# Performance work log

Measured on AMD Instinct MI355X. Metric: run time of the kernel, lower is better.

The kernel has to match this reference:

```python
import jax, jax.numpy as jnp
import numpy as np

EPS = 1e-8
LN_EPS = 1e-5
B, T, VDIM, ADIM, DM = 8, 2048, 1024, 768, 256
HID = 1024  # max(64, min(4*256, 2048))
DELTA_LOW, DELTA_HIGH = 2.0, 6.0
WINDOW = 5.0
GATE_MIN, GATE_MAX = 0.05, 0.95


def layer_norm(x):
    mu = jnp.mean(x, axis=-1, keepdims=True)
    var = jnp.var(x, axis=-1, keepdims=True)
    return (x - mu) / jnp.sqrt(var + LN_EPS)


def l2_normalize(x):
    n = jnp.sqrt(jnp.sum(x * x, axis=-1, keepdims=True))
    return x / jnp.maximum(n, EPS)


def setup_inputs() -> dict:
    key = jax.random.key(0)
    ks = jax.random.split(key, 8)
    inp = {
        "video_seq": jax.random.normal(ks[0], (B, T, VDIM), jnp.float32),
        "audio_seq": jax.random.normal(ks[1], (B, T, ADIM), jnp.float32),
        "Wv": jax.random.normal(ks[2], (VDIM, DM), jnp.float32) * (1.0 / np.sqrt(VDIM)),
        "bv": jnp.zeros((DM,), jnp.float32),
        "Wa": jax.random.normal(ks[3], (ADIM, DM), jnp.float32) * (1.0 / np.sqrt(ADIM)),
        "ba": jnp.zeros((DM,), jnp.float32),
        "theta": jnp.float32(0.0),
        "W1": jax.random.normal(ks[4], (3 * DM, HID), jnp.float32) * (1.0 / np.sqrt(3 * DM)),
        "b1": jnp.zeros((HID,), jnp.float32),
        "W2": jax.random.normal(ks[5], (HID, 1), jnp.float32) * (1.0 / np.sqrt(HID)),
        "b2": jnp.zeros((1,), jnp.float32),
    }
    return inp


def reference(video_seq, audio_seq, Wv, bv, Wa, ba, theta, W1, b1, W2, b2):
    v = layer_norm(video_seq @ Wv + bv)          # [B,T,DM]
    a = layer_norm(audio_seq @ Wa + ba)          # [B,T,DM]
    b, t, d = v.shape

    # LearnableDelay
    th = jnp.clip(theta, -12.0, 12.0)
    delta = DELTA_LOW + (DELTA_HIGH - DELTA_LOW) * jax.nn.sigmoid(th)
    delta_b = jnp.full((b,), delta, jnp.float32)

    # SoftTemporalShift (right shift with linear interpolation)
    dl = jnp.clip(delta_b, 0.0, float(t - 1))[:, None, None]   # [B,1,1]
    n = jnp.floor(dl)
    alpha = dl - n
    n_i = n.astype(jnp.int32)
    tidx = jnp.arange(t, dtype=jnp.int32)[None, :, None]       # [1,T,1]
    idx0 = jnp.clip(tidx - n_i, 0, t - 1)                      # [B,T,1]
    idx1 = jnp.clip(idx0 + 1, 0, t - 1)
    a0 = jnp.take_along_axis(a, jnp.broadcast_to(idx0, (b, t, d)), axis=1)
    a1 = jnp.take_along_axis(a, jnp.broadcast_to(idx1, (b, t, d)), axis=1)
    a_shift = (1.0 - alpha) * a0 + alpha * a1

    # DisplacementAwareCausalMask (hard, single scale)
    tf = jnp.arange(t, dtype=jnp.float32)
    tt = tf[None, :, None]                                     # t  -> [1,T,1]
    tau = tf[None, None, :]                                    # tau -> [1,1,T]
    center = jnp.minimum(jnp.maximum(tt + delta_b[:, None, None], 0.0), tt)
    raw = (jnp.abs(tau - center) <= WINDOW).astype(jnp.float32)
    raw = raw * (tau <= tt).astype(jnp.float32)
    M = raw / jnp.maximum(jnp.sum(raw, axis=-1, keepdims=True), EPS)  # [B,T,T]

    # mask-weighted audio context
    a_ctx = jnp.einsum('btk,bkd->btd', M, a_shift)

    # AlignmentGate (dropout inactive at eval)
    vn = l2_normalize(v)
    an = l2_normalize(a_ctx)
    x = jnp.concatenate([an, vn, an * vn], axis=-1)            # [B,T,3*DM]
    h = jax.nn.gelu(x @ W1 + b1, approximate=False)
    logits = jnp.clip(h @ W2 + b2, -12.0, 12.0)                # [B,T,1]
    g = jnp.clip(jax.nn.sigmoid(logits), GATE_MIN, GATE_MAX)

    fused = g * a_ctx + (1.0 - g) * v                          # [B,T,DM]
    return fused
```

## Files before the change

### kernel.cpp

```cpp
#include <hip/hip_runtime.h>
#include <cstdint>
#include <cstddef>

typedef unsigned short u16;
typedef unsigned int u32;
typedef __attribute__((ext_vector_type(8))) short short8;
typedef __attribute__((ext_vector_type(4))) float f32x4;

#define T_SEQ 2048
#define BT_ROWS 16384

__device__ __forceinline__ u16 f2bf(float x) {
  union { float f; u32 u; } v; v.f = x;
  u32 r = v.u + 0x7fffu + ((v.u >> 16) & 1u);
  return (u16)(r >> 16);
}
__device__ __forceinline__ u32 pkbf(float lo, float hi) {
  union { float f; u32 u; } a, b; a.f = lo; b.f = hi;
  const u32 ra = a.u + 0x7fffu + ((a.u >> 16) & 1u);
  const u32 rb = b.u + 0x7fffu + ((b.u >> 16) & 1u);
  return __builtin_amdgcn_perm(rb, ra, 0x07060302);
}
__device__ __forceinline__ float wave_bcast_sum(float x) {
#pragma unroll
  for (int off = 32; off > 0; off >>= 1) x += __shfl_down(x, off);
  return __shfl(x, 0);
}
__device__ __forceinline__ void gl_lds16(const void* g, void* l) {
  __builtin_amdgcn_global_load_lds((const __attribute__((address_space(1))) u32*)g,
                                   (__attribute__((address_space(3))) u32*)l, 16, 0, 0);
}
__device__ __forceinline__ float gelu_f(float x) {
  float z = 1.5957691216057308f * x * (1.0f + 0.044715f * x * x);
  float e = __expf(z);
  return x - x * __builtin_amdgcn_rcpf(1.0f + e);
}

__global__ __launch_bounds__(256) void tcvt_all(const float* __restrict__ Wv,
                                                const float* __restrict__ Wa,
                                                const float* __restrict__ W1,
                                                u16* __restrict__ wvT,
                                                u16* __restrict__ waT,
                                                u16* __restrict__ w1T,
                                                float* __restrict__ logits) {
  int b = blockIdx.x;
  if (b >= 1216) {
    logits[(b - 1216) * 256 + threadIdx.x] = 0.0f;
    return;
  }
  __shared__ float tile[32][33];
  const float* in; u16* out; int K, N, bx, by;
  if (b < 256)      { in = Wv; out = wvT; K = 1024; N = 256;  bx = b & 31;  by = b >> 5; }
  else if (b < 448) { b -= 256; in = Wa; out = waT; K = 768; N = 256;  bx = b % 24; by = b / 24; }
  else              { b -= 448; in = W1; out = w1T; K = 768; N = 1024; bx = b % 24; by = b / 24; }
  const int k0 = bx * 32, n0 = by * 32;
  const int tx = threadIdx.x & 31, ty = threadIdx.x >> 5;
#pragma unroll
  for (int r = 0; r < 4; r++)
    tile[ty + r * 8][tx] = in[(size_t)(k0 + ty + r * 8) * N + n0 + tx];
  __syncthreads();
#pragma unroll
  for (int r = 0; r < 4; r++)
    out[(size_t)(n0 + ty + r * 8) * K + k0 + tx] = f2bf(tile[tx][ty + r * 8]);
}

__global__ __launch_bounds__(256, 3) void proj_ln(const float* __restrict__ Vin,
                                                  const float* __restrict__ Ain,
                                                  const u16* __restrict__ wvT,
                                                  const u16* __restrict__ waT,
                                                  const float* __restrict__ bv,
                                                  const float* __restrict__ ba,
                                                  float* __restrict__ vOut,
                                                  float* __restrict__ aOut) {
  __shared__ float Asf[64 * 64];
  __shared__ u16 Bs[256 * 64];
  int b = blockIdx.x;
  const float* A; const u16* Bt; const float* bias; float* C; int K;
  if (b < 256) { A = Vin; Bt = wvT; bias = bv; C = vOut; K = 1024; }
  else         { b -= 256; A = Ain; Bt = waT; bias = ba; C = aOut; K = 768; }
  const int m0 = b * 64;
  const int tid = threadIdx.x;
  const int wave = tid >> 6, lane = tid & 63, qm = lane & 15, quad = lane >> 4;
  const int cw = wave * 64;

  const int arow = tid >> 4;
  const int apart = (tid & 15) ^ (arow & 15);
  const float* Ap[4];
#pragma unroll
  for (int g = 0; g < 4; g++)
    Ap[g] = A + (size_t)(m0 + arow + g * 16) * K + apart * 4;
  const int brow = tid >> 3;
  const int bpart = (tid & 7) ^ (brow & 7);
  const u16* Bp[8];
#pragma unroll
  for (int g = 0; g < 8; g++)
    Bp[g] = Bt + (size_t)(brow + g * 32) * K + bpart * 8;

  f32x4 acc[4][4] = {};
  for (int kt = 0; kt < K; kt += 64) {
#pragma unroll
    for (int g = 0; g < 4; g++) gl_lds16(Ap[g] + kt, &Asf[(tid + g * 256) * 4]);
#pragma unroll
    for (int g = 0; g < 8; g++) gl_lds16(Bp[g] + kt, &Bs[(tid + g * 256) * 8]);
    __syncthreads();
#pragma unroll
    for (int s = 0; s < 2; s++) {
      short8 af[4], bfr[4];
#pragma unroll
      for (int i = 0; i < 4; i++) {
        const int r = i * 16 + qm;
        const int pb = s * 8 + quad * 2;
        const float4 f0 = *(const float4*)&Asf[r * 64 + ((pb) ^ (r & 15)) * 4];
        const float4 f1 = *(const float4*)&Asf[r * 64 + ((pb + 1) ^ (r & 15)) * 4];
        u32 w[4] = {pkbf(f0.x, f0.y), pkbf(f0.z, f0.w), pkbf(f1.x, f1.y), pkbf(f1.z, f1.w)};
        af[i] = *(short8*)w;
      }
#pragma unroll
      for (int j = 0; j < 4; j++) {
        const int r = cw + j * 16 + qm;
        bfr[j] = *(const short8*)&Bs[r * 64 + ((s * 4 + quad) ^ (r & 7)) * 8];
      }
#pragma unroll
      for (int i = 0; i < 4; i++)
#pragma unroll
        for (int j = 0; j < 4; j++)
          acc[i][j] = __builtin_amdgcn_mfma_f32_16x16x32_bf16(af[i], bfr[j], acc[i][j], 0, 0, 0);
    }
    __syncthreads();
  }

  float bcol[4];
#pragma unroll
  for (int j = 0; j < 4; j++) bcol[j] = bias[cw + j * 16 + qm];
#pragma unroll
  for (int i = 0; i < 4; i++)
#pragma unroll
    for (int j = 0; j < 4; j++)
#pragma unroll
      for (int r = 0; r < 4; r++)
        acc[i][j][r] += bcol[j];
  float s1[4][4], s2[4][4];
#pragma unroll
  for (int i = 0; i < 4; i++)
#pragma unroll
    for (int r = 0; r < 4; r++) {
      float a1 = 0, a2 = 0;
#pragma unroll
      for (int j = 0; j < 4; j++) { a1 += acc[i][j][r]; a2 += acc[i][j][r] * acc[i][j][r]; }
#pragma unroll
      for (int off = 1; off < 16; off <<= 1) {
        a1 += __shfl_xor(a1, off);
        a2 += __shfl_xor(a2, off);
      }
      s1[i][r] = a1; s2[i][r] = a2;
    }
  float* red = Asf;
  if (qm == 0) {
#pragma unroll
    for (int i = 0; i < 4; i++)
#pragma unroll
      for (int r = 0; r < 4; r++) {
        const int row = i * 16 + quad * 4 + r;
        red[row * 8 + wave * 2] = s1[i][r];
        red[row * 8 + wave * 2 + 1] = s2[i][r];
      }
  }
  __syncthreads();
#pragma unroll
  for (int i = 0; i < 4; i++)
#pragma unroll
    for (int r = 0; r < 4; r++) {
      const int row = i * 16 + quad * 4 + r;
      const float4 q1 = *(const float4*)&red[row * 8];
      const float4 q2 = *(const float4*)&red[row * 8 + 4];
      const float st = q1.x + q1.z + q2.x + q2.z;
      const float st2 = q1.y + q1.w + q2.y + q2.w;
      const float mu = st * (1.0f / 256.0f);
      const float var = st2 * (1.0f / 256.0f) - mu * mu;
      const float inv = rsqrtf(var + 1e-5f);
#pragma unroll
      for (int j = 0; j < 4; j++)
        C[(size_t)(m0 + row) * 256 + cw + j * 16 + qm] = (acc[i][j][r] - mu) * inv;
    }
}

__global__ __launch_bounds__(256, 3) void gemm_gelu_w2(const u16* __restrict__ Axb,
                                                       const u16* __restrict__ Bt,
                                                       const float* __restrict__ b1,
                                                       const float* __restrict__ W2,
                                                       float* __restrict__ logits) {
  constexpr int K = 768;
  __shared__ u16 As[128 * 64];
  __shared__ u16 Bs[128 * 64];
  const int tid = threadIdx.x;
  const int n0 = blockIdx.x * 128;
  const int m0 = blockIdx.y * 128;
  const int wave = tid >> 6, lane = tid & 63, qm = lane & 15, quad = lane >> 4;
  const int rw = (wave >> 1) * 64, cw = (wave & 1) * 64;

  const int crow = tid >> 3;
  const int cpart = (tid & 7) ^ (crow & 7);
  const u16* Ap[4];
  const u16* Bp[4];
#pragma unroll
  for (int g = 0; g < 4; g++) {
    Ap[g] = Axb + (size_t)(m0 + crow + g * 32) * K + cpart * 8;
    Bp[g] = Bt + (size_t)(n0 + crow + g * 32) * K + cpart * 8;
  }

  f32x4 acc[4][4] = {};
  for (int kt = 0; kt < K; kt += 64) {
#pragma unroll
    for (int g = 0; g < 4; g++) gl_lds16(Ap[g] + kt, &As[(tid + g * 256) * 8]);
#pragma unroll
    for (int g = 0; g < 4; g++) gl_lds16(Bp[g] + kt, &Bs[(tid + g * 256) * 8]);
    __syncthreads();
#pragma unroll
    for (int s = 0; s < 2; s++) {
      short8 af[4], bfr[4];
#pragma unroll
      for (int i = 0; i < 4; i++) {
        const int r = rw + i * 16 + qm;
        af[i] = *(const short8*)&As[r * 64 + ((s * 4 + quad) ^ (r & 7)) * 8];
      }
#pragma unroll
      for (int j = 0; j < 4; j++) {
        const int r = cw + j * 16 + qm;
        bfr[j] = *(const short8*)&Bs[r * 64 + ((s * 4 + quad) ^ (r & 7)) * 8];
      }
#pragma unroll
      for (int i = 0; i < 4; i++)
#pragma unroll
        for (int j = 0; j < 4; j++)
          acc[i][j] = __builtin_amdgcn_mfma_f32_16x16x32_bf16(af[i], bfr[j], acc[i][j], 0, 0, 0);
    }
    __syncthreads();
  }

  float w2j[4], bc[4];
#pragma unroll
  for (int j = 0; j < 4; j++) {
    const int col = n0 + cw + j * 16 + qm;
    w2j[j] = W2[col];
    bc[j] = b1[col];
  }
#pragma unroll
  for (int i = 0; i < 4; i++) {
#pragma unroll
    for (int r = 0; r < 4; r++) {
      float p = 0.0f;
#pragma unroll
      for (int j = 0; j < 4; j++)
        p += gelu_f(acc[i][j][r] + bc[j]) * w2j[j];
      p += __shfl_xor(p, 1);
      p += __shfl_xor(p, 2);
      p += __shfl_xor(p, 4);
      p += __shfl_xor(p, 8);
      if (qm == 0)
        atomicAdd(&logits[m0 + rw + i * 16 + quad * 4 + r], p);
    }
  }
}

__global__ __launch_bounds__(256) void shift_norm(const float* __restrict__ a,
                                                  const float* __restrict__ v,
                                                  float* __restrict__ actx,
                                                  u16* __restrict__ xb,
                                                  const float* __restrict__ theta) {
  const int row = blockIdx.x * 4 + (threadIdx.x >> 6);
  const int lane = threadIdx.x & 63;
  const int d4 = lane * 4;
  const int bb = row >> 11;
  const int t = row & (T_SEQ - 1);
  const float th = fminf(fmaxf(theta[0], -12.0f), 12.0f);
  const float delta = 2.0f + 4.0f * (1.0f / (1.0f + expf(-th)));
  const float dl = fminf(fmaxf(delta, 0.0f), (float)(T_SEQ - 1));
  const float nf = floorf(dl);
  const float alpha = dl - nf;
  const int ni = (int)nf;
  const float center = fminf(fmaxf((float)t + delta, 0.0f), (float)t);
  float sx = 0, sy = 0, sz = 0, sw = 0, cnt = 0.0f;
  const float* ab = a + (size_t)bb * T_SEQ * 256;
#pragma unroll
  for (int j = 0; j < 6; j++) {
    const int tau = t - 5 + j;
    if (tau < 0) continue;
    if (fabsf((float)tau - center) > 5.0f) continue;
    cnt += 1.0f;
    const int i0 = min(max(tau - ni, 0), T_SEQ - 1);
    const int i1 = min(i0 + 1, T_SEQ - 1);
    const float4 a0 = *(const float4*)&ab[(size_t)i0 * 256 + d4];
    const float4 a1 = *(const float4*)&ab[(size_t)i1 * 256 + d4];
    sx += a0.x + alpha * (a1.x - a0.x);
    sy += a0.y + alpha * (a1.y - a0.y);
    sz += a0.z + alpha * (a1.z - a0.z);
    sw += a0.w + alpha * (a1.w - a0.w);
  }
  const float sc = 1.0f / fmaxf(cnt, 1e-8f);
  float4 o; o.x = sx * sc; o.y = sy * sc; o.z = sz * sc; o.w = sw * sc;
  *(float4*)&actx[(size_t)row * 256 + d4] = o;
  const float4 vv = *(const float4*)&v[(size_t)row * 256 + d4];
  float sa2 = o.x * o.x + o.y * o.y + o.z * o.z + o.w * o.w;
  float sv2 = vv.x * vv.x + vv.y * vv.y + vv.z * vv.z + vv.w * vv.w;
  sa2 = wave_bcast_sum(sa2);
  sv2 = wave_bcast_sum(sv2);
  const float ia = 1.0f / fmaxf(sqrtf(sa2), 1e-8f);
  const float iv = 1.0f / fmaxf(sqrtf(sv2), 1e-8f);
  const float anx = o.x * ia, any_ = o.y * ia, anz = o.z * ia, anw = o.w * ia;
  const float vnx = vv.x * iv, vny = vv.y * iv, vnz = vv.z * iv, vnw = vv.w * iv;
  u16* xr = xb + (size_t)row * 768;
  u32 pa[2] = {pkbf(anx, any_), pkbf(anz, anw)};
  u32 pv[2] = {pkbf(vnx, vny), pkbf(vnz, vnw)};
  u32 pp[2] = {pkbf(anx * vnx, any_ * vny), pkbf(anz * vnz, anw * vnw)};
  *(uint2*)&xr[d4] = *(uint2*)pa;
  *(uint2*)&xr[256 + d4] = *(uint2*)pv;
  *(uint2*)&xr[512 + d4] = *(uint2*)pp;
}

__global__ __launch_bounds__(256) void gate_mix(const float* __restrict__ logits,
                                                const float* __restrict__ b2,
                                                const float* __restrict__ actx,
                                                const float* __restrict__ v,
                                                float* __restrict__ out) {
  const int row = blockIdx.x * 4 + (threadIdx.x >> 6);
  const int lane = threadIdx.x & 63;
  const float l = fminf(fmaxf(logits[row] + b2[0], -12.0f), 12.0f);
  float g = 1.0f / (1.0f + expf(-l));
  g = fminf(fmaxf(g, 0.05f), 0.95f);
  const float4 aa = *(const float4*)&actx[(size_t)row * 256 + lane * 4];
  const float4 vv = *(const float4*)&v[(size_t)row * 256 + lane * 4];
  float4 o;
  o.x = g * aa.x + (1.0f - g) * vv.x;
  o.y = g * aa.y + (1.0f - g) * vv.y;
  o.z = g * aa.z + (1.0f - g) * vv.z;
  o.w = g * aa.w + (1.0f - g) * vv.w;
  *(float4*)&out[(size_t)row * 256 + lane * 4] = o;
}

extern "C" void kernel_launch(void* const* d_in, const int* in_sizes, int n_in,
                              void* d_out, int out_size, void* d_ws, size_t ws_size,
                              hipStream_t stream) {
  const float* video = (const float*)d_in[0];
  const float* audio = (const float*)d_in[1];
  const float* Wv    = (const float*)d_in[2];
  const float* bv    = (const float*)d_in[3];
  const float* Wa    = (const float*)d_in[4];
  const float* ba    = (const float*)d_in[5];
  const float* theta = (const float*)d_in[6];
  const float* W1    = (const float*)d_in[7];
  const float* b1    = (const float*)d_in[8];
  const float* W2    = (const float*)d_in[9];
  const float* b2    = (const float*)d_in[10];
  float* out = (float*)d_out;
  char* ws = (char*)d_ws;

  const size_t OFF_WVT = 0;
  const size_t OFF_WAT = 524288;
  const size_t OFF_W1T = 917504;
  const size_t OFF_LOG = 2490368;
  const size_t OFF_V   = 2555904;
  const size_t OFF_A   = 19333120;
  const size_t OFF_ACTX= 36110336;
  const size_t OFF_XB  = 52887552;

  u16* wvT = (u16*)(ws + OFF_WVT);
  u16* waT = (u16*)(ws + OFF_WAT);
  u16* w1T = (u16*)(ws + OFF_W1T);
  float* logits = (float*)(ws + OFF_LOG);
  float* v    = (float*)(ws + OFF_V);
  float* a    = (float*)(ws + OFF_A);
  float* actx = (float*)(ws + OFF_ACTX);
  u16* xb = (u16*)(ws + OFF_XB);

  tcvt_all<<<1280, 256, 0, stream>>>(Wv, Wa, W1, wvT, waT, w1T, logits);
  proj_ln<<<512, 256, 0, stream>>>(video, audio, wvT, waT, bv, ba, v, a);
  shift_norm<<<BT_ROWS / 4, 256, 0, stream>>>(a, v, actx, xb, theta);
  gemm_gelu_w2<<<dim3(8, BT_ROWS / 128), 256, 0, stream>>>(xb, w1T, b1, W2, logits);
  gate_mix<<<BT_ROWS / 4, 256, 0, stream>>>(logits, b2, actx, v, out);
}
```

Baseline: 244.1 us.

## Double-buffer proj_ln GEMM tiles and convert A to bf16 before LDS

The projection+LayerNorm GEMM now double-buffers its A and B shared-memory tiles. The next K-tile's global loads are issued before the MFMAs on the current tile, so only one barrier is needed per iteration. A is loaded into registers as fp32, converted to bf16 and stored to LDS in a swizzled layout, so the inner loop no longer repacks fp32 to bf16 on every fragment read. LDS use rises and occupancy bounds drop from 3 to 2 blocks per CU, trading occupancy for overlap.

```diff
diff --git a/kernel.cpp b/kernel.cpp
--- a/kernel.cpp
+++ b/kernel.cpp
@@ -64,7 +64,7 @@
     out[(size_t)(n0 + ty + r * 8) * K + k0 + tx] = f2bf(tile[tx][ty + r * 8]);
 }
 
-__global__ __launch_bounds__(256, 3) void proj_ln(const float* __restrict__ Vin,
+__global__ __launch_bounds__(256, 2) void proj_ln(const float* __restrict__ Vin,
                                                   const float* __restrict__ Ain,
                                                   const u16* __restrict__ wvT,
                                                   const u16* __restrict__ waT,
@@ -72,8 +72,8 @@
                                                   const float* __restrict__ ba,
                                                   float* __restrict__ vOut,
                                                   float* __restrict__ aOut) {
-  __shared__ float Asf[64 * 64];
-  __shared__ u16 Bs[256 * 64];
+  __shared__ __align__(16) u16 As[2][64 * 64];
+  __shared__ __align__(16) u16 Bs[2][256 * 64];
   int b = blockIdx.x;
   const float* A; const u16* Bt; const float* bias; float* C; int K;
   if (b < 256) { A = Vin; Bt = wvT; bias = bv; C = vOut; K = 1024; }
@@ -83,12 +83,14 @@
   const int wave = tid >> 6, lane = tid & 63, qm = lane & 15, quad = lane >> 4;
   const int cw = wave * 64;
 
-  const int arow = tid >> 4;
-  const int apart = (tid & 15) ^ (arow & 15);
-  const float* Ap[4];
-#pragma unroll
-  for (int g = 0; g < 4; g++)
-    Ap[g] = A + (size_t)(m0 + arow + g * 16) * K + apart * 4;
+  const int ar = tid >> 2;
+  const float* Arow = A + (size_t)(m0 + ar) * K + (tid & 3) * 4;
+  int awAddr[4];
+#pragma unroll
+  for (int g = 0; g < 4; g++) {
+    const int cg = ((tid & 3) >> 1) + 2 * g;
+    awAddr[g] = ar * 64 + ((cg ^ (ar & 7)) * 8) + (tid & 1) * 4;
+  }
   const int brow = tid >> 3;
   const int bpart = (tid & 7) ^ (brow & 7);
   const u16* Bp[8];
@@ -97,28 +99,45 @@
     Bp[g] = Bt + (size_t)(brow + g * 32) * K + bpart * 8;
 
   f32x4 acc[4][4] = {};
+
+  {
+    float4 p[4];
+#pragma unroll
+    for (int g = 0; g < 4; g++) p[g] = *(const float4*)(Arow + g * 16);
+#pragma unroll
+    for (int g = 0; g < 8; g++) gl_lds16(Bp[g], &Bs[0][(tid + g * 256) * 8]);
+#pragma unroll
+    for (int g = 0; g < 4; g++) {
+      uint2 w; w.x = pkbf(p[g].x, p[g].y); w.y = pkbf(p[g].z, p[g].w);
+      *(uint2*)&As[0][awAddr[g]] = w;
+    }
+  }
+  __syncthreads();
+
+  int cur = 0;
   for (int kt = 0; kt < K; kt += 64) {
-#pragma unroll
-    for (int g = 0; g < 4; g++) gl_lds16(Ap[g] + kt, &Asf[(tid + g * 256) * 4]);
-#pragma unroll
-    for (int g = 0; g < 8; g++) gl_lds16(Bp[g] + kt, &Bs[(tid + g * 256) * 8]);
-    __syncthreads();
+    const int nxt = cur ^ 1;
+    const int ktn = kt + 64;
+    const bool more = ktn < K;
+    float4 p[4];
+    if (more) {
+#pragma unroll
+      for (int g = 0; g < 4; g++) p[g] = *(const float4*)(Arow + ktn + g * 16);
+#pragma unroll
+      for (int g = 0; g < 8; g++) gl_lds16(Bp[g] + ktn, &Bs[nxt][(tid + g * 256) * 8]);
+    }
 #pragma unroll
     for (int s = 0; s < 2; s++) {
       short8 af[4], bfr[4];
 #pragma unroll
       for (int i = 0; i < 4; i++) {
         const int r = i * 16 + qm;
-        const int pb = s * 8 + quad * 2;
-        const float4 f0 = *(const float4*)&Asf[r * 64 + ((pb) ^ (r & 15)) * 4];
-        const float4 f1 = *(const float4*)&Asf[r * 64 + ((pb + 1) ^ (r & 15)) * 4];
-        u32 w[4] = {pkbf(f0.x, f0.y), pkbf(f0.z, f0.w), pkbf(f1.x, f1.y), pkbf(f1.z, f1.w)};
-        af[i] = *(short8*)w;
+        af[i] = *(const short8*)&As[cur][r * 64 + ((s * 4 + quad) ^ (r & 7)) * 8];
       }
 #pragma unroll
       for (int j = 0; j < 4; j++) {
         const int r = cw + j * 16 + qm;
-        bfr[j] = *(const short8*)&Bs[r * 64 + ((s * 4 + quad) ^ (r & 7)) * 8];
+        bfr[j] = *(const short8*)&Bs[cur][r * 64 + ((s * 4 + quad) ^ (r & 7)) * 8];
       }
 #pragma unroll
       for (int i = 0; i < 4; i++)
@@ -126,7 +145,15 @@
         for (int j = 0; j < 4; j++)
           acc[i][j] = __builtin_amdgcn_mfma_f32_16x16x32_bf16(af[i], bfr[j], acc[i][j], 0, 0, 0);
     }
+    if (more) {
+#pragma unroll
+      for (int g = 0; g < 4; g++) {
+        uint2 w; w.x = pkbf(p[g].x, p[g].y); w.y = pkbf(p[g].z, p[g].w);
+        *(uint2*)&As[nxt][awAddr[g]] = w;
+      }
+    }
     __syncthreads();
+    cur = nxt;
   }
 
   float bcol[4];
@@ -154,7 +181,7 @@
       }
       s1[i][r] = a1; s2[i][r] = a2;
     }
-  float* red = Asf;
+  float* red = (float*)As;
   if (qm == 0) {
 #pragma unroll
     for (int i = 0; i < 4; i++)
```

Result: no change. 244.3 us (+0.1%).
